# Performance work log

Measured on AMD Instinct MI355X. Metric: run time of the kernel, lower is better.

The kernel has to match this reference:

```python
import jax, jax.numpy as jnp
import numpy as np

B, N, S, VOCAB, D, NNZ = 16, 2048, 4096, 50257, 128, 1048576


def setup_inputs() -> dict:
    key = jax.random.key(0)
    k1, k2, k3, k4, k5, k6 = jax.random.split(key, 6)
    return {
        "subnode_ids": jax.random.randint(k1, (B, S), 0, VOCAB),
        "mask_batch": jax.random.randint(k2, (NNZ,), 0, B),
        "mask_node": jax.random.randint(k3, (NNZ,), 0, N),
        "mask_subnode": jax.random.randint(k4, (NNZ,), 0, S),
        "mask_values": jax.random.uniform(k5, (NNZ,), dtype=jnp.float32),
        "emb_table": jax.random.normal(k6, (VOCAB, D), dtype=jnp.float32),
    }


def reference(subnode_ids, mask_batch, mask_node, mask_subnode, mask_values, emb_table):
    # Gather token embeddings for every (batch, subnode) slot: [B, S, D] -> [B*S, D]
    subnode_emb = emb_table[subnode_ids].reshape(B * S, D)
    # Flattened COO indices (same as batch*max_nodes + node, batch*max_subnodes + subnode)
    row = mask_batch * N + mask_node      # destination node slot in [0, B*N)
    col = mask_batch * S + mask_subnode   # source subnode slot in [0, B*S)
    # Fused gather + weighted scatter-add (== sparse.mm of expanded_mask @ subnode_emb)
    contrib = subnode_emb[col] * mask_values[:, None]           # [NNZ, D]
    pooled = jax.ops.segment_sum(contrib, row, num_segments=B * N)  # [B*N, D]
    return pooled.reshape(B, N, D)
```

## Files before the change

kernel.cpp:

```cpp
#include <hip/hip_runtime.h>
#include <hip/hip_fp16.h>

#define Bq 16
#define Nq 2048
#define Sq 4096
#define Dq 128
#define VOCABq 50257
#define NNZq 1048576
#define ROWS (Bq * Nq)
#define NBIN 512
#define RPB 64
#define BTPB 1024
#define BEPT 4
#define ENT (BTPB * BEPT)
#define NBLK (NNZq / ENT)
#define PTPB 512
#define NKEY 256
#define EBUF 2560
#define NQUAD ((VOCABq * Dq) / 4)

typedef unsigned long long u64;
typedef u64 u64x2 __attribute__((ext_vector_type(2)));
typedef float vfloat4 __attribute__((ext_vector_type(4)));
typedef unsigned short vushort4 __attribute__((ext_vector_type(4)));
typedef unsigned short vushort8 __attribute__((ext_vector_type(8)));

template <int NW>
__device__ __forceinline__ int scan_block(int val, int t, int* waveSum) {
    int lane = t & 63, wid = t >> 6;
    int vi = val;
    #pragma unroll
    for (int d = 1; d < 64; d <<= 1) {
        int w = __shfl_up(vi, d, 64);
        if (lane >= d) vi += w;
    }
    if (lane == 63) waveSum[wid] = vi;
    __syncthreads();
    if (t == 0) {
        int s = 0;
        #pragma unroll
        for (int w = 0; w < NW; w++) { int x = waveSum[w]; waveSum[w] = s; s += x; }
    }
    __syncthreads();
    return vi - val + waveSum[wid];
}

#define FMA8(e_, v_, A0_, A1_)                                   \
    A0_.x += __half2float(__ushort_as_half(e_[0])) * v_;         \
    A0_.y += __half2float(__ushort_as_half(e_[1])) * v_;         \
    A0_.z += __half2float(__ushort_as_half(e_[2])) * v_;         \
    A0_.w += __half2float(__ushort_as_half(e_[3])) * v_;         \
    A1_.x += __half2float(__ushort_as_half(e_[4])) * v_;         \
    A1_.y += __half2float(__ushort_as_half(e_[5])) * v_;         \
    A1_.z += __half2float(__ushort_as_half(e_[6])) * v_;         \
    A1_.w += __half2float(__ushort_as_half(e_[7])) * v_;

__device__ __forceinline__ void accum_range(
    const u64* ebuf, int k, int s1, int lane16,
    const unsigned short* __restrict__ emb16, vfloat4& A0, vfloat4& A1)
{
    for (; k + 8 <= s1; k += 8) {
        int tk[8]; float vv[8];
        #pragma unroll
        for (int u = 0; u < 8; u++) {
            u64 pk = ebuf[k + u];
            tk[u] = (int)(pk & 0xFFFF);
            vv[u] = __int_as_float((int)(pk >> 32));
        }
        vushort8 e[8];
        #pragma unroll
        for (int u = 0; u < 8; u++)
            e[u] = reinterpret_cast<const vushort8*>(emb16 + (size_t)tk[u] * Dq)[lane16];
        #pragma unroll
        for (int u = 0; u < 8; u++) { FMA8(e[u], vv[u], A0, A1) }
    }
    int rem = s1 - k;
    if (rem > 0) {
        int tk[8]; float vv[8]; vushort8 e[8];
        #pragma unroll
        for (int u = 0; u < 8; u++) if (u < rem) {
            u64 pk = ebuf[k + u];
            tk[u] = (int)(pk & 0xFFFF);
            vv[u] = __int_as_float((int)(pk >> 32));
        }
        #pragma unroll
        for (int u = 0; u < 8; u++) if (u < rem)
            e[u] = reinterpret_cast<const vushort8*>(emb16 + (size_t)tk[u] * Dq)[lane16];
        #pragma unroll
        for (int u = 0; u < 8; u++) if (u < rem) { FMA8(e[u], vv[u], A0, A1) }
    }
}

__device__ __forceinline__ void accum_pair(
    const u64* ebuf, int ka, int s1a, int kb, int s1b, int lane16,
    const unsigned short* __restrict__ emb16,
    vfloat4& A0, vfloat4& A1, vfloat4& B0, vfloat4& B1)
{
    while (ka + 8 <= s1a && kb + 8 <= s1b) {
        int tk[16]; float vv[16];
        #pragma unroll
        for (int u = 0; u < 8; u++) {
            u64 pa = ebuf[ka + u];
            tk[u]     = (int)(pa & 0xFFFF);
            vv[u]     = __int_as_float((int)(pa >> 32));
            u64 pb = ebuf[kb + u];
            tk[u + 8] = (int)(pb & 0xFFFF);
            vv[u + 8] = __int_as_float((int)(pb >> 32));
        }
        vushort8 e[16];
        #pragma unroll
        for (int u = 0; u < 16; u++)
            e[u] = reinterpret_cast<const vushort8*>(emb16 + (size_t)tk[u] * Dq)[lane16];
        #pragma unroll
        for (int u = 0; u < 8; u++) { FMA8(e[u], vv[u], A0, A1) }
        #pragma unroll
        for (int u = 0; u < 8; u++) { FMA8(e[u + 8], vv[u + 8], B0, B1) }
        ka += 8; kb += 8;
    }
    accum_range(ebuf, ka, s1a, lane16, emb16, A0, A1);
    accum_range(ebuf, kb, s1b, lane16, emb16, B0, B1);
}

__global__ __launch_bounds__(256) void cast_kernel(
    const float* __restrict__ emb, unsigned short* __restrict__ emb16)
{
    int i = blockIdx.x * 256 + threadIdx.x;
    if (i >= NQUAD) return;
    vfloat4 f = reinterpret_cast<const vfloat4*>(emb)[i];
    vushort4 h;
    h.x = __half_as_ushort(__float2half_rn(f.x));
    h.y = __half_as_ushort(__float2half_rn(f.y));
    h.z = __half_as_ushort(__float2half_rn(f.z));
    h.w = __half_as_ushort(__float2half_rn(f.w));
    __builtin_nontemporal_store(h, reinterpret_cast<vushort4*>(emb16) + i);
}

__global__ __launch_bounds__(BTPB) void bin_kernel(
    const int* __restrict__ subnode_ids,
    const int* __restrict__ mb,
    const int* __restrict__ mn,
    const int* __restrict__ ms,
    const float* __restrict__ mv,
    u64* __restrict__ binMem,
    unsigned* __restrict__ offTab)
{
    __shared__ int hist[NBIN];
    __shared__ int lstart[NBIN];
    __shared__ int waveSum[BTPB / 64];
    __shared__ u64 spk[ENT] __attribute__((aligned(16)));

    int t   = threadIdx.x;
    int blk = blockIdx.x;

    if (t < NBIN) hist[t] = 0;
    __syncthreads();

    int base = blk * ENT;
    int g[BEPT], rank[BEPT];
    u64 pk[BEPT];
    #pragma unroll
    for (int k = 0; k < BEPT; k++) {
        int i   = base + k * BTPB + t;
        int b   = __builtin_nontemporal_load(mb + i);
        int row = b * Nq + __builtin_nontemporal_load(mn + i);
        int s   = __builtin_nontemporal_load(ms + i);
        float v = __builtin_nontemporal_load(mv + i);
        int tok = subnode_ids[b * Sq + s];
        g[k]  = row >> 6;
        pk[k] = ((u64)(unsigned)__float_as_int(v) << 32)
              | ((u64)(row & 63) << 16)
              | (unsigned)tok;
        rank[k] = atomicAdd(&hist[g[k]], 1);
    }
    __syncthreads();

    int cnt = (t < NBIN) ? hist[t] : 0;
    int ex  = scan_block<BTPB / 64>(cnt, t, waveSum);
    if (t < NBIN) {
        lstart[t] = ex;
        offTab[blk * NBIN + t] = (unsigned)ex | ((unsigned)cnt << 16);
    }
    __syncthreads();

    #pragma unroll
    for (int k = 0; k < BEPT; k++)
        spk[lstart[g[k]] + rank[k]] = pk[k];
    __syncthreads();

    const u64x2* s2 = reinterpret_cast<const u64x2*>(spk);
    u64x2* d2 = reinterpret_cast<u64x2*>(binMem + (size_t)blk * ENT);
    #pragma unroll
    for (int p = t; p < ENT / 2; p += BTPB) d2[p] = s2[p];
}

__global__ __launch_bounds__(PTPB) void pool_kernel(
    const unsigned short* __restrict__ emb16,
    const u64* __restrict__ binMem,
    const unsigned* __restrict__ offTab,
    float* __restrict__ out)
{
    __shared__ u64 spk[EBUF] __attribute__((aligned(16)));
    __shared__ u64 ebuf[EBUF];
    __shared__ int waveSum[PTPB / 64];
    __shared__ int khist[NKEY];
    __shared__ int kstart[NKEY + 1];
    __shared__ int kcursor[NKEY];
    __shared__ int nTot;

    int t   = threadIdx.x;
    int bin = blockIdx.x;

    int slice = t >> 1, half = t & 1;
    unsigned m = offTab[slice * NBIN + bin];
    int soff = (int)(m & 0xFFFFu);
    int c    = (int)(m >> 16);
    int c0   = (c + 1) >> 1;
    int myoff = soff + (half ? c0 : 0);
    int myc   = half ? (c - c0) : c0;
    int db = scan_block<PTPB / 64>(myc, t, waveSum);
    if (t == PTPB - 1) nTot = db + myc;
    if (db >= EBUF) myc = 0;
    else if (db + myc > EBUF) myc = EBUF - db;

    {
        const u64* src = binMem + (size_t)slice * ENT + myoff;
        for (int i = 0; i < myc; i++) spk[db + i] = src[i];
    }
    if (t < NKEY) khist[t] = 0;
    __syncthreads();

    int n = nTot < EBUF ? nTot : EBUF;

    for (int e = t; e < n; e += PTPB) {
        u64 p = spk[e];
        int key = (((int)(p & 0xFFFF)) >> 14 << 6) | ((int)(p >> 16) & 63);
        atomicAdd(&khist[key], 1);
    }
    __syncthreads();

    int kval = (t < NKEY) ? khist[t] : 0;
    int kex  = scan_block<PTPB / 64>(kval, t, waveSum);
    if (t < NKEY) {
        kstart[t]  = kex;
        kcursor[t] = kex;
        if (t == NKEY - 1) kstart[NKEY] = kex + kval;
    }
    __syncthreads();

    for (int e = t; e < n; e += PTPB) {
        u64 p = spk[e];
        int key = (((int)(p & 0xFFFF)) >> 14 << 6) | ((int)(p >> 16) & 63);
        int pos = atomicAdd(&kcursor[key], 1);
        ebuf[pos] = p;
    }
    __syncthreads();

    int g2     = t >> 4;
    int lane16 = t & 15;
    int r0 = g2, r1 = g2 + 32;
    vfloat4 a0 = {0.f,0.f,0.f,0.f}, a1 = {0.f,0.f,0.f,0.f};
    vfloat4 b0 = {0.f,0.f,0.f,0.f}, b1 = {0.f,0.f,0.f,0.f};
    #pragma unroll
    for (int q = 0; q < 4; q++) {
        accum_pair(ebuf,
                   kstart[q * 64 + r0], kstart[q * 64 + r0 + 1],
                   kstart[q * 64 + r1], kstart[q * 64 + r1 + 1],
                   lane16, emb16, a0, a1, b0, b1);
    }

    float* orow0 = out + ((size_t)bin * RPB + r0) * Dq + lane16 * 8;
    float* orow1 = out + ((size_t)bin * RPB + r1) * Dq + lane16 * 8;
    __builtin_nontemporal_store(a0, reinterpret_cast<vfloat4*>(orow0));
    __builtin_nontemporal_store(a1, reinterpret_cast<vfloat4*>(orow0) + 1);
    __builtin_nontemporal_store(b0, reinterpret_cast<vfloat4*>(orow1));
    __builtin_nontemporal_store(b1, reinterpret_cast<vfloat4*>(orow1) + 1);
}

extern "C" void kernel_launch(void* const* d_in, const int* in_sizes, int n_in,
                              void* d_out, int out_size, void* d_ws, size_t ws_size,
                              hipStream_t stream) {
    const int*   subnode_ids  = (const int*)d_in[0];
    const int*   mask_batch   = (const int*)d_in[1];
    const int*   mask_node    = (const int*)d_in[2];
    const int*   mask_subnode = (const int*)d_in[3];
    const float* mask_values  = (const float*)d_in[4];
    const float* emb_table    = (const float*)d_in[5];
    float*       out          = (float*)d_out;

    unsigned short* emb16 = (unsigned short*)d_ws;
    u64* binMem = (u64*)(emb16 + (size_t)VOCABq * Dq + 64 );
    unsigned* offTab = (unsigned*)(binMem + (size_t)NBLK * ENT);

    cast_kernel<<<(NQUAD + 255) / 256, 256, 0, stream>>>(emb_table, emb16);
    bin_kernel<<<NBLK, BTPB, 0, stream>>>(
        subnode_ids, mask_batch, mask_node, mask_subnode, mask_values,
        binMem, offTab);
    pool_kernel<<<NBIN, PTPB, 0, stream>>>(emb16, binMem, offTab, out);
}
```

Measured before the change: 133.4 us.

## Pre-bin entries by token quarter and process pool bins in four LDS-light passes

The bin kernel now keys its histogram by row group and the top two bits of the token, so entries arrive pre-split into four token-range quarters. The pool kernel processes each quarter in its own pass, using much smaller shared buffers sized to 768 entries. The pool kernel also declares an occupancy hint of 8 in its launch bounds. The aim is to cut LDS use to raise occupancy and to improve embedding-table cache locality within each pass. In exchange it adds four rounds of block syncs and scans per bin, drops the paired 16-wide gather loop in favour of accum_range, and silently truncates any quarter above the buffer capacity.

New measurement: 207.8 us. 55.7% more time.

```diff
diff --git a/kernel.cpp b/kernel.cpp
--- a/kernel.cpp
+++ b/kernel.cpp
@@ -14,14 +14,15 @@
 #define BEPT 4
 #define ENT (BTPB * BEPT)
 #define NBLK (NNZq / ENT)
+#define NKEY2 2048
 #define PTPB 512
-#define NKEY 256
-#define EBUF 2560
+#define QCAP 768
 #define NQUAD ((VOCABq * Dq) / 4)
 
 typedef unsigned long long u64;
 typedef u64 u64x2 __attribute__((ext_vector_type(2)));
 typedef float vfloat4 __attribute__((ext_vector_type(4)));
+typedef unsigned vuint4 __attribute__((ext_vector_type(4)));
 typedef unsigned short vushort4 __attribute__((ext_vector_type(4)));
 typedef unsigned short vushort8 __attribute__((ext_vector_type(8)));
 
@@ -91,36 +92,6 @@
     }
 }
 
-__device__ __forceinline__ void accum_pair(
-    const u64* ebuf, int ka, int s1a, int kb, int s1b, int lane16,
-    const unsigned short* __restrict__ emb16,
-    vfloat4& A0, vfloat4& A1, vfloat4& B0, vfloat4& B1)
-{
-    while (ka + 8 <= s1a && kb + 8 <= s1b) {
-        int tk[16]; float vv[16];
-        #pragma unroll
-        for (int u = 0; u < 8; u++) {
-            u64 pa = ebuf[ka + u];
-            tk[u]     = (int)(pa & 0xFFFF);
-            vv[u]     = __int_as_float((int)(pa >> 32));
-            u64 pb = ebuf[kb + u];
-            tk[u + 8] = (int)(pb & 0xFFFF);
-            vv[u + 8] = __int_as_float((int)(pb >> 32));
-        }
-        vushort8 e[16];
-        #pragma unroll
-        for (int u = 0; u < 16; u++)
-            e[u] = reinterpret_cast<const vushort8*>(emb16 + (size_t)tk[u] * Dq)[lane16];
-        #pragma unroll
-        for (int u = 0; u < 8; u++) { FMA8(e[u], vv[u], A0, A1) }
-        #pragma unroll
-        for (int u = 0; u < 8; u++) { FMA8(e[u + 8], vv[u + 8], B0, B1) }
-        ka += 8; kb += 8;
-    }
-    accum_range(ebuf, ka, s1a, lane16, emb16, A0, A1);
-    accum_range(ebuf, kb, s1b, lane16, emb16, B0, B1);
-}
-
 __global__ __launch_bounds__(256) void cast_kernel(
     const float* __restrict__ emb, unsigned short* __restrict__ emb16)
 {
@@ -144,15 +115,16 @@
     u64* __restrict__ binMem,
     unsigned* __restrict__ offTab)
 {
-    __shared__ int hist[NBIN];
-    __shared__ int lstart[NBIN];
+    __shared__ int hist[NKEY2];
+    __shared__ int lstart[NKEY2];
     __shared__ int waveSum[BTPB / 64];
     __shared__ u64 spk[ENT] __attribute__((aligned(16)));
 
     int t   = threadIdx.x;
     int blk = blockIdx.x;
 
-    if (t < NBIN) hist[t] = 0;
+    hist[2 * t]     = 0;
+    hist[2 * t + 1] = 0;
     __syncthreads();
 
     int base = blk * ENT;
@@ -166,7 +138,7 @@
         int s   = __builtin_nontemporal_load(ms + i);
         float v = __builtin_nontemporal_load(mv + i);
         int tok = subnode_ids[b * Sq + s];
-        g[k]  = row >> 6;
+        g[k]  = ((row >> 6) << 2) | (tok >> 14);
         pk[k] = ((u64)(unsigned)__float_as_int(v) << 32)
               | ((u64)(row & 63) << 16)
               | (unsigned)tok;
@@ -174,12 +146,12 @@
     }
     __syncthreads();
 
-    int cnt = (t < NBIN) ? hist[t] : 0;
-    int ex  = scan_block<BTPB / 64>(cnt, t, waveSum);
-    if (t < NBIN) {
-        lstart[t] = ex;
-        offTab[blk * NBIN + t] = (unsigned)ex | ((unsigned)cnt << 16);
-    }
+    int v0 = hist[2 * t], v1 = hist[2 * t + 1];
+    int ex = scan_block<BTPB / 64>(v0 + v1, t, waveSum);
+    lstart[2 * t]     = ex;
+    lstart[2 * t + 1] = ex + v0;
+    offTab[(size_t)blk * NKEY2 + 2 * t]     = (unsigned)ex        | ((unsigned)v0 << 16);
+    offTab[(size_t)blk * NKEY2 + 2 * t + 1] = (unsigned)(ex + v0) | ((unsigned)v1 << 16);
     __syncthreads();
 
     #pragma unroll
@@ -193,83 +165,82 @@
     for (int p = t; p < ENT / 2; p += BTPB) d2[p] = s2[p];
 }
 
-__global__ __launch_bounds__(PTPB) void pool_kernel(
+__global__ __launch_bounds__(PTPB, 8) void pool_kernel(
     const unsigned short* __restrict__ emb16,
     const u64* __restrict__ binMem,
     const unsigned* __restrict__ offTab,
     float* __restrict__ out)
 {
-    __shared__ u64 spk[EBUF] __attribute__((aligned(16)));
-    __shared__ u64 ebuf[EBUF];
+    __shared__ u64 spkQ[QCAP] __attribute__((aligned(16)));
+    __shared__ u64 ebufQ[QCAP];
     __shared__ int waveSum[PTPB / 64];
-    __shared__ int khist[NKEY];
-    __shared__ int kstart[NKEY + 1];
-    __shared__ int kcursor[NKEY];
+    __shared__ int khist[64];
+    __shared__ int kstart[65];
+    __shared__ int kcursor[64];
     __shared__ int nTot;
 
     int t   = threadIdx.x;
     int bin = blockIdx.x;
 
-    int slice = t >> 1, half = t & 1;
-    unsigned m = offTab[slice * NBIN + bin];
-    int soff = (int)(m & 0xFFFFu);
-    int c    = (int)(m >> 16);
-    int c0   = (c + 1) >> 1;
-    int myoff = soff + (half ? c0 : 0);
-    int myc   = half ? (c - c0) : c0;
-    int db = scan_block<PTPB / 64>(myc, t, waveSum);
-    if (t == PTPB - 1) nTot = db + myc;
-    if (db >= EBUF) myc = 0;
-    else if (db + myc > EBUF) myc = EBUF - db;
-
-    {
-        const u64* src = binMem + (size_t)slice * ENT + myoff;
-        for (int i = 0; i < myc; i++) spk[db + i] = src[i];
-    }
-    if (t < NKEY) khist[t] = 0;
-    __syncthreads();
-
-    int n = nTot < EBUF ? nTot : EBUF;
-
-    for (int e = t; e < n; e += PTPB) {
-        u64 p = spk[e];
-        int key = (((int)(p & 0xFFFF)) >> 14 << 6) | ((int)(p >> 16) & 63);
-        atomicAdd(&khist[key], 1);
-    }
-    __syncthreads();
-
-    int kval = (t < NKEY) ? khist[t] : 0;
-    int kex  = scan_block<PTPB / 64>(kval, t, waveSum);
-    if (t < NKEY) {
-        kstart[t]  = kex;
-        kcursor[t] = kex;
-        if (t == NKEY - 1) kstart[NKEY] = kex + kval;
-    }
-    __syncthreads();
-
-    for (int e = t; e < n; e += PTPB) {
-        u64 p = spk[e];
-        int key = (((int)(p & 0xFFFF)) >> 14 << 6) | ((int)(p >> 16) & 63);
-        int pos = atomicAdd(&kcursor[key], 1);
-        ebuf[pos] = p;
-    }
-    __syncthreads();
+    vuint4 mm = {0, 0, 0, 0};
+    if (t < NBLK)
+        mm = *reinterpret_cast<const vuint4*>(offTab + (size_t)t * NKEY2 + bin * 4);
 
     int g2     = t >> 4;
     int lane16 = t & 15;
-    int r0 = g2, r1 = g2 + 32;
     vfloat4 a0 = {0.f,0.f,0.f,0.f}, a1 = {0.f,0.f,0.f,0.f};
     vfloat4 b0 = {0.f,0.f,0.f,0.f}, b1 = {0.f,0.f,0.f,0.f};
+
     #pragma unroll
     for (int q = 0; q < 4; q++) {
-        accum_pair(ebuf,
-                   kstart[q * 64 + r0], kstart[q * 64 + r0 + 1],
-                   kstart[q * 64 + r1], kstart[q * 64 + r1 + 1],
-                   lane16, emb16, a0, a1, b0, b1);
-    }
-
-    float* orow0 = out + ((size_t)bin * RPB + r0) * Dq + lane16 * 8;
-    float* orow1 = out + ((size_t)bin * RPB + r1) * Dq + lane16 * 8;
+        unsigned m = (q == 0) ? mm.x : (q == 1) ? mm.y : (q == 2) ? mm.z : mm.w;
+        int soff = (int)(m & 0xFFFFu);
+        int c    = (t < NBLK) ? (int)(m >> 16) : 0;
+        int db   = scan_block<PTPB / 64>(c, t, waveSum);
+        if (t == PTPB - 1) nTot = db + c;
+        if (db >= QCAP) c = 0;
+        else if (db + c > QCAP) c = QCAP - db;
+        if (t < 64) khist[t] = 0;
+        __syncthreads();
+        int n = nTot < QCAP ? nTot : QCAP;
+
+        if (c > 0) {
+            const u64* src = binMem + (size_t)t * ENT + soff;
+            for (int i = 0; i < c; i++) spkQ[db + i] = src[i];
+        }
+        __syncthreads();
+
+        for (int e = t; e < n; e += PTPB)
+            atomicAdd(&khist[(int)(spkQ[e] >> 16) & 63], 1);
+        __syncthreads();
+
+        if (t < 64) {
+            int v  = khist[t];
+            int vi = v;
+            #pragma unroll
+            for (int d = 1; d < 64; d <<= 1) {
+                int w = __shfl_up(vi, d, 64);
+                if (t >= d) vi += w;
+            }
+            kstart[t + 1] = vi;
+            kcursor[t]    = vi - v;
+            if (t == 0) kstart[0] = 0;
+        }
+        __syncthreads();
+
+        for (int e = t; e < n; e += PTPB) {
+            u64 p = spkQ[e];
+            int pos = atomicAdd(&kcursor[(int)(p >> 16) & 63], 1);
+            ebufQ[pos] = p;
+        }
+        __syncthreads();
+
+        accum_range(ebufQ, kstart[g2],      kstart[g2 + 1],  lane16, emb16, a0, a1);
+        accum_range(ebufQ, kstart[g2 + 32], kstart[g2 + 33], lane16, emb16, b0, b1);
+    }
+
+    float* orow0 = out + ((size_t)bin * RPB + g2) * Dq + lane16 * 8;
+    float* orow1 = out + ((size_t)bin * RPB + g2 + 32) * Dq + lane16 * 8;
     __builtin_nontemporal_store(a0, reinterpret_cast<vfloat4*>(orow0));
     __builtin_nontemporal_store(a1, reinterpret_cast<vfloat4*>(orow0) + 1);
     __builtin_nontemporal_store(b0, reinterpret_cast<vfloat4*>(orow1));
```
